# Kernel optimization log

Hardware: AMD Instinct MI355X
Metric: run time of the kernel (lower is better)

The kernel has to match this reference:

```python
import jax, jax.numpy as jnp
import numpy as np

H = 512  # hidden_size


def setup_inputs() -> dict:
    key = jax.random.key(0)
    k1, k2, k3, k4, k5 = jax.random.split(key, 5)
    B, S = 32, 2048
    hidden = jax.random.normal(k1, (1, B, H), dtype=jnp.float32)
    encoder_outputs = jax.random.normal(k2, (B, S, 2 * H), dtype=jnp.float32)
    # nn.Linear(3H, H): weight [H, 3H], store transposed [3H, H] for x @ W
    scale_a = 1.0 / np.sqrt(3 * H)
    Wa = jax.random.uniform(k3, (3 * H, H), jnp.float32, -scale_a, scale_a)
    ba = jax.random.uniform(k4, (H,), jnp.float32, -scale_a, scale_a)
    # nn.Linear(H, 1, bias=False): weight [1, H] -> store as [H]
    scale_v = 1.0 / np.sqrt(H)
    v = jax.random.uniform(k5, (H,), jnp.float32, -scale_v, scale_v)
    return {"hidden": hidden, "encoder_outputs": encoder_outputs,
            "Wa": Wa, "ba": ba, "v": v}


def reference(hidden, encoder_outputs, Wa, ba, v):
    # hidden: [1, B, H] -> [B, H]; encoder_outputs: [B, S, 2H]
    h = jnp.squeeze(hidden, axis=0)                      # [B, H]
    # Split concat-linear into two projections (same math as cat + matmul):
    Wh, We = Wa[:H], Wa[H:]                              # [H, H], [2H, H]
    # energy: [B, S, H] = tanh(h Wh + enc We + b), h broadcast over S
    energy = jnp.tanh(h @ Wh + jnp.einsum('bse,eh->bsh', encoder_outputs, We)[..., :, :] + ba) if False else \
             jnp.tanh((h @ Wh)[:, None, :] + jnp.einsum('bse,eh->bsh', encoder_outputs, We) + ba)
    scores = jnp.einsum('bsh,h->bs', energy, v)          # [B, S]
    attention_weights = jax.nn.softmax(scores, axis=1)   # [B, S]
    context = jnp.einsum('bs,bse->be', attention_weights, encoder_outputs)  # [B, 2H]
    return context, attention_weights
```

## Files before the change

kernel.cpp:

```cpp
#include <hip/hip_runtime.h>

typedef unsigned short ushort_t;
typedef __attribute__((ext_vector_type(8))) short bf16x8;
typedef __attribute__((ext_vector_type(4))) float f32x4;

#define H 512
#define E 1024
#define S 2048
#define B 32
#define NCHUNK (S / 64)

__device__ __forceinline__ ushort_t f2bf(float f) {
    unsigned u = __float_as_uint(f);
    unsigned r = (u + 0x7FFFu + ((u >> 16) & 1u)) >> 16;
    return (ushort_t)r;
}

__device__ __forceinline__ unsigned pkbf(float x, float y) {
    unsigned u0 = __float_as_uint(x) + 0x8000u;
    unsigned u1 = __float_as_uint(y) + 0x8000u;
    return __builtin_amdgcn_perm(u1, u0, 0x07060302u);
}

__device__ __forceinline__ float fast_tanh(float x) {
    float e = __expf(2.f * x);
    return 1.f - 2.f / (e + 1.f);
}

__global__ void prep_hb(const float* __restrict__ hidden, const float* __restrict__ Wa,
                        const float* __restrict__ ba, float* __restrict__ hb) {
    int b = blockIdx.x, kc = blockIdx.y, tid = threadIdx.x;
    const float* hp = hidden + b * H + kc * 64;
    float a0 = 0.f, a1 = 0.f;
    #pragma unroll 8
    for (int k = 0; k < 64; ++k) {
        float hv = hp[k];
        a0 += hv * Wa[(size_t)(kc * 64 + k) * H + tid];
        a1 += hv * Wa[(size_t)(kc * 64 + k) * H + tid + 256];
    }
    if (kc == 0) { a0 += ba[tid]; a1 += ba[tid + 256]; }
    atomicAdd(&hb[b * H + tid], a0);
    atomicAdd(&hb[b * H + tid + 256], a1);
}

__global__ void prep_wef(const float* __restrict__ Wa, ushort_t* __restrict__ wef) {
    int g = blockIdx.x * 256 + threadIdx.x;
    int kt = g >> 11, nt = (g >> 6) & 31, l = g & 63;
    int kbase = kt * 32 + ((l >> 4) << 3);
    int n = nt * 16 + (l & 15);
    #pragma unroll
    for (int j = 0; j < 8; ++j)
        wef[(size_t)g * 8 + j] = f2bf(Wa[(size_t)(H + kbase + j) * H + n]);
}

__launch_bounds__(256, 2)
__global__ void score_kernel(const float* __restrict__ enc, const ushort_t* __restrict__ wef,
                             const float* __restrict__ hb, const float* __restrict__ v,
                             float* __restrict__ scores, float* __restrict__ mpart,
                             float* __restrict__ lpart, float* __restrict__ ctxp) {
    int sc = blockIdx.x;
    int b = blockIdx.y;
    int s0 = sc * 64;
    int tid = threadIdx.x;
    int wave = tid >> 6, lane = tid & 63;
    int q = lane >> 4, nl = lane & 15;

    __shared__ char arena[32768];
    float* sred = (float*)arena;
    float* lds_p = (float*)arena + 256;

    f32x4 acc[4][8] = {};
    bf16x8 bregA[8], bregB[8];

    int r0 = wave * 16 + (lane >> 3);
    int c4 = ((lane & 7) ^ (lane >> 3)) * 4;
    const float* asrc0 = enc + ((size_t)b * S + s0 + r0) * E + c4;
    const float* asrc1 = asrc0 + 8 * E;
    const bf16x8* bsrc = (const bf16x8*)wef + (size_t)(wave * 8) * 64 + lane;

#define STAGE_A(KT)                                                                      \
    {                                                                                    \
        char* al = arena + ((KT) & 3) * 8192 + wave * 2048;                              \
        __builtin_amdgcn_global_load_lds(                                                \
            (const __attribute__((address_space(1))) unsigned*)(asrc0 + (KT) * 32),      \
            (__attribute__((address_space(3))) unsigned*)(al), 16, 0, 0);                \
        __builtin_amdgcn_global_load_lds(                                                \
            (const __attribute__((address_space(1))) unsigned*)(asrc1 + (KT) * 32),      \
            (__attribute__((address_space(3))) unsigned*)(al + 1024), 16, 0, 0);         \
    }

#define LOADB(BREG, KT)                                                                  \
    _Pragma("unroll")                                                                    \
    for (int ntl = 0; ntl < 8; ++ntl) BREG[ntl] = bsrc[(size_t)(KT) * 2048 + ntl * 64];

#define COMPUTE(KT, BREG)                                                                \
    {                                                                                    \
        const float* Ac = (const float*)(arena + ((KT) & 3) * 8192);                     \
        bf16x8 afr[4];                                                                   \
        _Pragma("unroll")                                                                \
        for (int mt = 0; mt < 4; ++mt) {                                                 \
            int r = mt * 16 + nl;                                                        \
            int sa = r * 8 + ((2 * q) ^ (nl & 7));                                       \
            int sb = r * 8 + ((2 * q + 1) ^ (nl & 7));                                   \
            float4 f0 = *(const float4*)(Ac + sa * 4);                                   \
            float4 f1 = *(const float4*)(Ac + sb * 4);                                   \
            uint4 u;                                                                     \
            u.x = pkbf(f0.x, f0.y); u.y = pkbf(f0.z, f0.w);                              \
            u.z = pkbf(f1.x, f1.y); u.w = pkbf(f1.z, f1.w);                              \
            afr[mt] = *(bf16x8*)&u;                                                      \
        }                                                                                \
        _Pragma("unroll")                                                                \
        for (int ntl = 0; ntl < 8; ++ntl) {                                              \
            _Pragma("unroll")                                                            \
            for (int mt = 0; mt < 4; ++mt)                                               \
                acc[mt][ntl] = __builtin_amdgcn_mfma_f32_16x16x32_bf16(                  \
                    afr[mt], BREG[ntl], acc[mt][ntl], 0, 0, 0);                          \
        }                                                                                \
    }

    STAGE_A(0);
    STAGE_A(1);
    __builtin_amdgcn_sched_barrier(0);
    LOADB(bregA, 0);
    __builtin_amdgcn_sched_barrier(0);
    asm volatile("s_waitcnt vmcnt(10)" ::: "memory");
    __builtin_amdgcn_s_barrier();
    __builtin_amdgcn_sched_barrier(0);

#define FULL_ITER(T, BCUR, BNEXT)                                                        \
    STAGE_A((T) + 2);                                                                    \
    __builtin_amdgcn_sched_barrier(0);                                                   \
    LOADB(BNEXT, (T) + 1);                                                               \
    COMPUTE((T), BCUR);                                                                  \
    __builtin_amdgcn_sched_barrier(0);                                                   \
    asm volatile("s_waitcnt vmcnt(10)" ::: "memory");                                    \
    __builtin_amdgcn_s_barrier();                                                        \
    __builtin_amdgcn_sched_barrier(0);

    for (int it = 0; it < 15; ++it) {
        FULL_ITER(it * 2, bregA, bregB);
        FULL_ITER(it * 2 + 1, bregB, bregA);
    }
    LOADB(bregB, 31);
    COMPUTE(30, bregA);
    __builtin_amdgcn_sched_barrier(0);
    asm volatile("s_waitcnt vmcnt(8)" ::: "memory");
    __builtin_amdgcn_s_barrier();
    __builtin_amdgcn_sched_barrier(0);
    COMPUTE(31, bregB);
    __syncthreads();

    float p[16];
    #pragma unroll
    for (int i = 0; i < 16; ++i) p[i] = 0.f;
    #pragma unroll
    for (int ntl = 0; ntl < 8; ++ntl) {
        int n = wave * 128 + ntl * 16 + nl;
        float hv = hb[b * H + n];
        float vv = v[n];
        #pragma unroll
        for (int mt = 0; mt < 4; ++mt)
            #pragma unroll
            for (int r = 0; r < 4; ++r)
                p[mt * 4 + r] += vv * fast_tanh(acc[mt][ntl][r] + hv);
    }
    #pragma unroll
    for (int off = 1; off < 16; off <<= 1) {
        #pragma unroll
        for (int i = 0; i < 16; ++i) p[i] += __shfl_xor(p[i], off, 64);
    }
    if (nl == 0) {
        #pragma unroll
        for (int mt = 0; mt < 4; ++mt)
            #pragma unroll
            for (int r = 0; r < 4; ++r)
                sred[wave * 64 + mt * 16 + q * 4 + r] = p[mt * 4 + r];
    }
    __syncthreads();

    if (tid < 64) {
        float s = sred[tid] + sred[64 + tid] + sred[128 + tid] + sred[192 + tid];
        scores[(size_t)b * S + s0 + tid] = s;
        float m = s;
        #pragma unroll
        for (int off = 32; off; off >>= 1) m = fmaxf(m, __shfl_xor(m, off, 64));
        float pe = __expf(s - m);
        lds_p[tid] = pe;
        float l = pe;
        #pragma unroll
        for (int off = 32; off; off >>= 1) l += __shfl_xor(l, off, 64);
        if (tid == 0) { mpart[b * NCHUNK + sc] = m; lpart[b * NCHUNK + sc] = l; }
    }
    __syncthreads();

    const float* ep = enc + ((size_t)b * S + s0) * E + tid * 4;
    float cx = 0.f, cy = 0.f, cz = 0.f, cw = 0.f;
    #pragma unroll 8
    for (int s = 0; s < 64; ++s) {
        float ps = lds_p[s];
        float4 x = *(const float4*)(ep + (size_t)s * E);
        cx += ps * x.x; cy += ps * x.y; cz += ps * x.z; cw += ps * x.w;
    }
    float4 co = {cx, cy, cz, cw};
    *(float4*)(ctxp + ((size_t)(b * NCHUNK + sc)) * E + tid * 4) = co;
#undef STAGE_A
#undef LOADB
#undef COMPUTE
#undef FULL_ITER
}

__global__ void combine_kernel(const float* __restrict__ scores, const float* __restrict__ mpart,
                               const float* __restrict__ lpart, const float* __restrict__ ctxp,
                               float* __restrict__ out) {
    int b = blockIdx.x, tid = threadIdx.x;
    __shared__ float sscale[NCHUNK];
    __shared__ float sml[2];
    if (tid < NCHUNK) {
        float m = mpart[b * NCHUNK + tid];
        float M = m;
        #pragma unroll
        for (int off = 16; off; off >>= 1) M = fmaxf(M, __shfl_xor(M, off, 64));
        float e = __expf(m - M);
        float l = lpart[b * NCHUNK + tid] * e;
        float L = l;
        #pragma unroll
        for (int off = 16; off; off >>= 1) L += __shfl_xor(L, off, 64);
        sscale[tid] = e;
        if (tid == 0) { sml[0] = M; sml[1] = L; }
    }
    __syncthreads();
    float M = sml[0], invL = 1.0f / sml[1];
    int e0 = tid * 4;
    float cx = 0.f, cy = 0.f, cz = 0.f, cw = 0.f;
    #pragma unroll 4
    for (int i = 0; i < NCHUNK; ++i) {
        float scv = sscale[i];
        float4 x = *(const float4*)(ctxp + ((size_t)(b * NCHUNK + i)) * E + e0);
        cx += scv * x.x; cy += scv * x.y; cz += scv * x.z; cw += scv * x.w;
    }
    float4 co = {cx * invL, cy * invL, cz * invL, cw * invL};
    *(float4*)(out + (size_t)b * E + e0) = co;
    const float* srow = scores + (size_t)b * S;
    float* wrow = out + B * E + (size_t)b * S;
    #pragma unroll
    for (int j = 0; j < 8; ++j) {
        int s = tid + j * 256;
        wrow[s] = __expf(srow[s] - M) * invL;
    }
}

extern "C" void kernel_launch(void* const* d_in, const int* in_sizes, int n_in,
                              void* d_out, int out_size, void* d_ws, size_t ws_size,
                              hipStream_t stream) {
    const float* hidden = (const float*)d_in[0];
    const float* enc    = (const float*)d_in[1];
    const float* Wa     = (const float*)d_in[2];
    const float* ba     = (const float*)d_in[3];
    const float* v      = (const float*)d_in[4];
    float* out = (float*)d_out;

    char* ws = (char*)d_ws;
    ushort_t* wef = (ushort_t*)ws;
    float* hb     = (float*)(ws + (1 << 20));
    float* scores = (float*)(ws + (1 << 20) + (1 << 16));
    float* mpart  = (float*)(ws + (1 << 20) + (1 << 16) + (1 << 18));
    float* lpart  = mpart + B * NCHUNK;
    float* ctxp   = (float*)(ws + (1 << 20) + (1 << 16) + (1 << 18) + (1 << 14));

    hipMemsetAsync(hb, 0, B * H * sizeof(float), stream);
    prep_hb<<<dim3(B, 8), 256, 0, stream>>>(hidden, Wa, ba, hb);
    prep_wef<<<256, 256, 0, stream>>>(Wa, wef);
    score_kernel<<<dim3(NCHUNK, B), 256, 0, stream>>>(enc, wef, hb, v,
                                                      scores, mpart, lpart, ctxp);
    combine_kernel<<<B, 256, 0, stream>>>(scores, mpart, lpart, ctxp, out);
}
```

Baseline: 455.5 us.

## Give each wave a private double-buffered A tile to drop block barriers

```diff
diff --git a/kernel.cpp b/kernel.cpp
--- a/kernel.cpp
+++ b/kernel.cpp
@@ -65,28 +65,28 @@
     int wave = tid >> 6, lane = tid & 63;
     int q = lane >> 4, nl = lane & 15;
 
-    __shared__ char arena[32768];
+    __shared__ char arena[65536];
+    char* wbuf = arena + wave * 16384;
     float* sred = (float*)arena;
     float* lds_p = (float*)arena + 256;
 
     f32x4 acc[4][8] = {};
     bf16x8 bregA[8], bregB[8];
 
-    int r0 = wave * 16 + (lane >> 3);
+    int r0 = lane >> 3;
     int c4 = ((lane & 7) ^ (lane >> 3)) * 4;
-    const float* asrc0 = enc + ((size_t)b * S + s0 + r0) * E + c4;
-    const float* asrc1 = asrc0 + 8 * E;
+    const float* asrc = enc + ((size_t)b * S + s0 + r0) * E + c4;
     const bf16x8* bsrc = (const bf16x8*)wef + (size_t)(wave * 8) * 64 + lane;
 
 #define STAGE_A(KT)                                                                      \
     {                                                                                    \
-        char* al = arena + ((KT) & 3) * 8192 + wave * 2048;                              \
-        __builtin_amdgcn_global_load_lds(                                                \
-            (const __attribute__((address_space(1))) unsigned*)(asrc0 + (KT) * 32),      \
-            (__attribute__((address_space(3))) unsigned*)(al), 16, 0, 0);                \
-        __builtin_amdgcn_global_load_lds(                                                \
-            (const __attribute__((address_space(1))) unsigned*)(asrc1 + (KT) * 32),      \
-            (__attribute__((address_space(3))) unsigned*)(al + 1024), 16, 0, 0);         \
+        char* al = wbuf + ((KT) & 1) * 8192;                                             \
+        _Pragma("unroll")                                                                \
+        for (int j = 0; j < 8; ++j)                                                      \
+            __builtin_amdgcn_global_load_lds(                                            \
+                (const __attribute__((address_space(1))) unsigned*)                      \
+                    (asrc + (size_t)(KT) * 32 + j * 8 * E),                              \
+                (__attribute__((address_space(3))) unsigned*)(al + j * 1024), 16, 0, 0); \
     }
 
 #define LOADB(BREG, KT)                                                                  \
@@ -95,7 +95,7 @@
 
 #define COMPUTE(KT, BREG)                                                                \
     {                                                                                    \
-        const float* Ac = (const float*)(arena + ((KT) & 3) * 8192);                     \
+        const float* Ac = (const float*)(wbuf + ((KT) & 1) * 8192);                      \
         bf16x8 afr[4];                                                                   \
         _Pragma("unroll")                                                                \
         for (int mt = 0; mt < 4; ++mt) {                                                 \
@@ -119,33 +119,25 @@
     }
 
     STAGE_A(0);
-    STAGE_A(1);
     __builtin_amdgcn_sched_barrier(0);
     LOADB(bregA, 0);
     __builtin_amdgcn_sched_barrier(0);
-    asm volatile("s_waitcnt vmcnt(10)" ::: "memory");
-    __builtin_amdgcn_s_barrier();
-    __builtin_amdgcn_sched_barrier(0);
 
 #define FULL_ITER(T, BCUR, BNEXT)                                                        \
-    STAGE_A((T) + 2);                                                                    \
+    STAGE_A((T) + 1);                                                                    \
     __builtin_amdgcn_sched_barrier(0);                                                   \
     LOADB(BNEXT, (T) + 1);                                                               \
-    COMPUTE((T), BCUR);                                                                  \
     __builtin_amdgcn_sched_barrier(0);                                                   \
-    asm volatile("s_waitcnt vmcnt(10)" ::: "memory");                                    \
-    __builtin_amdgcn_s_barrier();                                                        \
-    __builtin_amdgcn_sched_barrier(0);
+    asm volatile("s_waitcnt vmcnt(24)" ::: "memory");                                    \
+    __builtin_amdgcn_sched_barrier(0);                                                   \
+    COMPUTE((T), BCUR);
 
     for (int it = 0; it < 15; ++it) {
         FULL_ITER(it * 2, bregA, bregB);
         FULL_ITER(it * 2 + 1, bregB, bregA);
     }
-    LOADB(bregB, 31);
-    COMPUTE(30, bregA);
-    __builtin_amdgcn_sched_barrier(0);
+    FULL_ITER(30, bregA, bregB);
     asm volatile("s_waitcnt vmcnt(8)" ::: "memory");
-    __builtin_amdgcn_s_barrier();
     __builtin_amdgcn_sched_barrier(0);
     COMPUTE(31, bregB);
     __syncthreads();
```

New measurement: 463.1 us. No clear change (+1.7%).
